# Kernel tuning notes

Measured on AMD Instinct MI355X. Metric: run time of the kernel, lower is better.

## Reference

```python
import jax, jax.numpy as jnp
import numpy as np
from jax import lax

_K1 = np.array([[0,0,0,0,0],[0,-1,2,-1,0],[0,2,4,2,0],[0,-1,2,-1,0],[0,0,0,0,0]], dtype=np.float32)
_K2 = np.array([[-1,2,-2,2,-1],[2,-6,8,-6,2],[-2,8,-12,8,-2],[2,-6,8,-6,2],[-1,2,-2,2,-1]], dtype=np.float32)
_K3 = np.array([[0,0,0,0,0],[0,0,0,0,0],[0,1,-2,1,0],[0,0,0,0,0],[0,0,0,0,0]], dtype=np.float32)

def _depthwise_filter(k, C):
    # OIHW with feature_group_count=C -> (C, 1, 5, 5)
    return jnp.broadcast_to(jnp.asarray(k)[None, None], (C, 1, 5, 5))

def _dwconv(x, f):
    C = x.shape[1]
    return lax.conv_general_dilated(
        x, f, window_strides=(1, 1), padding=[(2, 2), (2, 2)],
        dimension_numbers=('NCHW', 'OIHW', 'NCHW'), feature_group_count=C)

def setup_inputs() -> dict:
    key = jax.random.key(0)
    x = jax.random.normal(key, (64, 3, 512, 512), dtype=jnp.float32)
    return {"x": x}

def reference(x):
    C = x.shape[1]
    f1 = _depthwise_filter(_K1, C)
    f2 = _depthwise_filter(_K2, C)
    f3 = _depthwise_filter(_K3, C)
    edge = _dwconv(x, f1)
    texture = _dwconv(edge, f2)
    residual = _dwconv(texture, f3)
    return residual
```

## Files before the change

### kernel.cpp

```cpp
#include <hip/hip_runtime.h>


#define H 512
#define W 512
#define RS 16
#define STRIPS (H/RS)
#define LOG2_STRIPS 5

typedef float v4f __attribute__((ext_vector_type(4)));

__global__ __launch_bounds__(256, 4)
void resid_kernel(const float* __restrict__ x, float* __restrict__ out) {
    const int lane  = threadIdx.x & 63;
    const int wid   = (blockIdx.x << 2) | (threadIdx.x >> 6);
    const int plane = wid >> LOG2_STRIPS;
    const int strip = wid & (STRIPS - 1);
    const int r0    = strip * RS;
    const int cb    = lane << 3;

    const float* __restrict__ xp = x + (size_t)plane * (H * W);
    float* __restrict__ op = out + (size_t)plane * (H * W);

    float E0[8], E1[8], E2[8], E3[8], E4[8];
    float a0[8], a1[8];
    #pragma unroll
    for (int j = 0; j < 8; ++j) {
        E0[j] = E1[j] = E2[j] = E3[j] = E4[j] = 0.f;
        a0[j] = a1[j] = 0.f;
    }

    for (int r = r0 - 3; r <= r0 + RS + 3; ++r) {
        float v[8], vl, vh;
        if (r >= 0 && r < H) {
            const float4* pr = (const float4*)(xp + r * W + cb);
            float4 qa = pr[0], qb = pr[1];
            v[0] = qa.x; v[1] = qa.y; v[2] = qa.z; v[3] = qa.w;
            v[4] = qb.x; v[5] = qb.y; v[6] = qb.z; v[7] = qb.w;
            vl = (lane > 0)  ? xp[r * W + cb - 1] : 0.f;
            vh = (lane < 63) ? xp[r * W + cb + 8] : 0.f;
        } else {
            #pragma unroll
            for (int j = 0; j < 8; ++j) v[j] = 0.f;
            vl = 0.f; vh = 0.f;
        }

        if (r >= r0 + 4) {
            const int p = r - 4;
            float A[8], B[8];
            #pragma unroll
            for (int j = 0; j < 8; ++j) {
                A[j] = E0[j] - 2.f*E1[j] + 2.f*E2[j] - 2.f*E3[j] + E4[j];
                B[j] = E1[j] - 2.f*E2[j] + E3[j];
            }
            float al1 = __shfl_up(A[7], 1, 64);
            float al2 = __shfl_up(A[6], 1, 64);
            float ah1 = __shfl_down(A[0], 1, 64);
            float ah2 = __shfl_down(A[1], 1, 64);
            float bl  = __shfl_up(B[7], 1, 64);
            float bh  = __shfl_down(B[0], 1, 64);
            if (lane == 0)  { al1 = 0.f; al2 = 0.f; bl = 0.f; }
            if (lane == 63) { ah1 = 0.f; ah2 = 0.f; bh = 0.f; }
            float T[8];
            #pragma unroll
            for (int j = 0; j < 8; ++j) {
                float am2 = (j >= 2) ? A[j-2] : ((j == 1) ? al1 : al2);
                float am1 = (j >= 1) ? A[j-1] : al1;
                float ap1 = (j <= 6) ? A[j+1] : ah1;
                float ap2 = (j <= 5) ? A[j+2] : ((j == 6) ? ah1 : ah2);
                float bm  = (j >= 1) ? B[j-1] : bl;
                float bp  = (j <= 6) ? B[j+1] : bh;
                float lt = am2 - 2.f*am1 + 2.f*A[j] - 2.f*ap1 + ap2;
                float mt = bm - 2.f*B[j] + bp;
                T[j] = -lt - 2.f*mt;
            }
            float tl = __shfl_up(T[7], 1, 64);
            float th = __shfl_down(T[0], 1, 64);
            if (lane == 0)  tl = 0.f;
            if (lane == 63) th = 0.f;
            float R[8];
            #pragma unroll
            for (int j = 0; j < 8; ++j) {
                float tm = (j >= 1) ? T[j-1] : tl;
                float tp = (j <= 6) ? T[j+1] : th;
                R[j] = tm - 2.f*T[j] + tp;
            }
            v4f o0 = { R[0], R[1], R[2], R[3] };
            v4f o1 = { R[4], R[5], R[6], R[7] };
            float* dst = op + p * W + cb;
            __builtin_nontemporal_store(o0, (v4f*)(dst));
            __builtin_nontemporal_store(o1, (v4f*)(dst + 4));
        }

        const bool ein = (r - 1 >= 0) && (r - 1 < H);
        #pragma unroll
        for (int j = 0; j < 8; ++j) {
            float xm = (j >= 1) ? v[j-1] : vl;
            float xq = (j <= 6) ? v[j+1] : vh;
            float h1 = 2.f*v[j] - xm - xq;
            float h2 = 8.f*v[j] - 2.f*h1;
            float En = ein ? (a0[j] + h1) : 0.f;
            a0[j] = a1[j] + h2;
            a1[j] = h1;
            E0[j] = E1[j]; E1[j] = E2[j]; E2[j] = E3[j]; E3[j] = E4[j]; E4[j] = En;
        }
    }
}

extern "C" void kernel_launch(void* const* d_in, const int* in_sizes, int n_in,
                              void* d_out, int out_size, void* d_ws, size_t ws_size,
                              hipStream_t stream) {
    const float* x = (const float*)d_in[0];
    float* out = (float*)d_out;
    resid_kernel<<<dim3(1536), dim3(256), 0, stream>>>(x, out);
}
```

Measured before the change: 361.6 us.

## Fully unroll row loop into four-row groups with batched clamped loads

Replaces the per-row loop with a prologue and four unrolled groups of four rows. Each group issues all four row loads before computing, so more memory requests are in flight per wave. Loads now use clamped, branch-free row addresses and zero the values with selects instead of branching. The register-shifting E window is replaced by ping-pong register sets, and launch bounds drop from 4 to 3 to allow the extra registers, which lowers the occupancy floor.

```diff
diff --git a/kernel.cpp b/kernel.cpp
--- a/kernel.cpp
+++ b/kernel.cpp
@@ -9,7 +9,102 @@
 
 typedef float v4f __attribute__((ext_vector_type(4)));
 
-__global__ __launch_bounds__(256, 4)
+__device__ __forceinline__ void load_row(const float* __restrict__ xp, int r, int cb, int lane,
+                                         float v[8], float& lo, float& hi) {
+    int rc = r; if (rc < 0) rc = 0; if (rc > H - 1) rc = H - 1;
+    const float* rp = xp + rc * W;
+    v4f a = *(const v4f*)(rp + cb);
+    v4f b = *(const v4f*)(rp + cb + 4);
+    float l = rp[(lane == 0)  ? 0       : cb - 1];
+    float h = rp[(lane == 63) ? W - 1   : cb + 8];
+    const bool ok = (r >= 0) && (r < H);
+    v[0] = ok ? a.x : 0.f; v[1] = ok ? a.y : 0.f; v[2] = ok ? a.z : 0.f; v[3] = ok ? a.w : 0.f;
+    v[4] = ok ? b.x : 0.f; v[5] = ok ? b.y : 0.f; v[6] = ok ? b.z : 0.f; v[7] = ok ? b.w : 0.f;
+    lo = (ok && lane > 0)  ? l : 0.f;
+    hi = (ok && lane < 63) ? h : 0.f;
+}
+
+#define FOLD(xv, xl, xh, r, Eout, KEEP)                                   \
+  {                                                                       \
+    const bool eok = ((r) - 1 >= 0) && ((r) - 1 < H);                     \
+    _Pragma("unroll")                                                     \
+    for (int j = 0; j < 8; ++j) {                                         \
+      float xm = (j >= 1) ? xv[j-1] : xl;                                 \
+      float xq = (j <= 6) ? xv[j+1] : xh;                                 \
+      float h1 = 2.f*xv[j] - xm - xq;                                     \
+      float h2 = 8.f*xv[j] - 2.f*h1;                                      \
+      if (KEEP) Eout[j] = eok ? (a0[j] + h1) : 0.f;                       \
+      a0[j] = a1[j] + h2;                                                 \
+      a1[j] = h1;                                                         \
+    }                                                                     \
+  }
+
+#define OUTROW(p, Em2, Em1, Ez, Ep1, Ep2)                                 \
+  {                                                                       \
+    float A[8], B[8];                                                     \
+    _Pragma("unroll")                                                     \
+    for (int j = 0; j < 8; ++j) {                                         \
+      A[j] = Em2[j] - 2.f*Em1[j] + 2.f*Ez[j] - 2.f*Ep1[j] + Ep2[j];       \
+      B[j] = Em1[j] - 2.f*Ez[j] + Ep1[j];                                 \
+    }                                                                     \
+    float al1 = __shfl_up(A[7], 1, 64);                                   \
+    float al2 = __shfl_up(A[6], 1, 64);                                   \
+    float ah1 = __shfl_down(A[0], 1, 64);                                 \
+    float ah2 = __shfl_down(A[1], 1, 64);                                 \
+    float bl  = __shfl_up(B[7], 1, 64);                                   \
+    float bh  = __shfl_down(B[0], 1, 64);                                 \
+    if (lane == 0)  { al1 = 0.f; al2 = 0.f; bl = 0.f; }                   \
+    if (lane == 63) { ah1 = 0.f; ah2 = 0.f; bh = 0.f; }                   \
+    float T[8];                                                           \
+    _Pragma("unroll")                                                     \
+    for (int j = 0; j < 8; ++j) {                                         \
+      float am2 = (j >= 2) ? A[j-2] : ((j == 1) ? al1 : al2);             \
+      float am1 = (j >= 1) ? A[j-1] : al1;                                \
+      float ap1 = (j <= 6) ? A[j+1] : ah1;                                \
+      float ap2 = (j <= 5) ? A[j+2] : ((j == 6) ? ah1 : ah2);             \
+      float bm  = (j >= 1) ? B[j-1] : bl;                                 \
+      float bp  = (j <= 6) ? B[j+1] : bh;                                 \
+      float lt = am2 - 2.f*am1 + 2.f*A[j] - 2.f*ap1 + ap2;                \
+      float mt = bm - 2.f*B[j] + bp;                                      \
+      T[j] = -lt - 2.f*mt;                                                \
+    }                                                                     \
+    float tl = __shfl_up(T[7], 1, 64);                                    \
+    float th = __shfl_down(T[0], 1, 64);                                  \
+    if (lane == 0)  tl = 0.f;                                             \
+    if (lane == 63) th = 0.f;                                             \
+    float Rr[8];                                                          \
+    _Pragma("unroll")                                                     \
+    for (int j = 0; j < 8; ++j) {                                         \
+      float tm = (j >= 1) ? T[j-1] : tl;                                  \
+      float tp = (j <= 6) ? T[j+1] : th;                                  \
+      Rr[j] = tm - 2.f*T[j] + tp;                                         \
+    }                                                                     \
+    v4f o0 = { Rr[0], Rr[1], Rr[2], Rr[3] };                              \
+    v4f o1 = { Rr[4], Rr[5], Rr[6], Rr[7] };                              \
+    float* dst = op + (p) * W + cb;                                       \
+    __builtin_nontemporal_store(o0, (v4f*)(dst));                         \
+    __builtin_nontemporal_store(o1, (v4f*)(dst + 4));                     \
+  }
+
+#define GROUP(P, Oa, Ob, Oc, Od, Na, Nb, Nc, Nd)                          \
+  {                                                                       \
+    float xv0[8], xv1[8], xv2[8], xv3[8];                                 \
+    float xl0, xh0, xl1, xh1, xl2, xh2, xl3, xh3;                         \
+    load_row(xp, (P)+3, cb, lane, xv0, xl0, xh0);                         \
+    load_row(xp, (P)+4, cb, lane, xv1, xl1, xh1);                         \
+    load_row(xp, (P)+5, cb, lane, xv2, xl2, xh2);                         \
+    load_row(xp, (P)+6, cb, lane, xv3, xl3, xh3);                         \
+    FOLD(xv0, xl0, xh0, (P)+3, Na, true);                                 \
+    FOLD(xv1, xl1, xh1, (P)+4, Nb, true);                                 \
+    FOLD(xv2, xl2, xh2, (P)+5, Nc, true);                                 \
+    FOLD(xv3, xl3, xh3, (P)+6, Nd, true);                                 \
+    OUTROW((P),   Oa, Ob, Oc, Od, Na);                                    \
+    OUTROW((P)+1, Ob, Oc, Od, Na, Nb);                                    \
+    OUTROW((P)+2, Oc, Od, Na, Nb, Nc);                                    \
+    OUTROW((P)+3, Od, Na, Nb, Nc, Nd);                                    \
+  }
+
+__global__ __launch_bounds__(256, 3)
 void resid_kernel(const float* __restrict__ x, float* __restrict__ out) {
     const int lane  = threadIdx.x & 63;
     const int wid   = (blockIdx.x << 2) | (threadIdx.x >> 6);
@@ -21,89 +116,34 @@
     const float* __restrict__ xp = x + (size_t)plane * (H * W);
     float* __restrict__ op = out + (size_t)plane * (H * W);
 
-    float E0[8], E1[8], E2[8], E3[8], E4[8];
     float a0[8], a1[8];
     #pragma unroll
-    for (int j = 0; j < 8; ++j) {
-        E0[j] = E1[j] = E2[j] = E3[j] = E4[j] = 0.f;
-        a0[j] = a1[j] = 0.f;
+    for (int j = 0; j < 8; ++j) { a0[j] = 0.f; a1[j] = 0.f; }
+
+    float O0[8], O1[8], O2[8], O3[8];
+    float N0[8], N1[8], N2[8], N3[8];
+
+    {
+        float pv0[8], pv1[8], pv2[8], pv3[8], pv4[8], pv5[8];
+        float pl0, ph0, pl1, ph1, pl2, ph2, pl3, ph3, pl4, ph4, pl5, ph5;
+        load_row(xp, r0-3, cb, lane, pv0, pl0, ph0);
+        load_row(xp, r0-2, cb, lane, pv1, pl1, ph1);
+        load_row(xp, r0-1, cb, lane, pv2, pl2, ph2);
+        load_row(xp, r0,   cb, lane, pv3, pl3, ph3);
+        load_row(xp, r0+1, cb, lane, pv4, pl4, ph4);
+        load_row(xp, r0+2, cb, lane, pv5, pl5, ph5);
+        FOLD(pv0, pl0, ph0, r0-3, O0, false);
+        FOLD(pv1, pl1, ph1, r0-2, O0, false);
+        FOLD(pv2, pl2, ph2, r0-1, O0, true);
+        FOLD(pv3, pl3, ph3, r0,   O1, true);
+        FOLD(pv4, pl4, ph4, r0+1, O2, true);
+        FOLD(pv5, pl5, ph5, r0+2, O3, true);
     }
 
-    for (int r = r0 - 3; r <= r0 + RS + 3; ++r) {
-        float v[8], vl, vh;
-        if (r >= 0 && r < H) {
-            const float4* pr = (const float4*)(xp + r * W + cb);
-            float4 qa = pr[0], qb = pr[1];
-            v[0] = qa.x; v[1] = qa.y; v[2] = qa.z; v[3] = qa.w;
-            v[4] = qb.x; v[5] = qb.y; v[6] = qb.z; v[7] = qb.w;
-            vl = (lane > 0)  ? xp[r * W + cb - 1] : 0.f;
-            vh = (lane < 63) ? xp[r * W + cb + 8] : 0.f;
-        } else {
-            #pragma unroll
-            for (int j = 0; j < 8; ++j) v[j] = 0.f;
-            vl = 0.f; vh = 0.f;
-        }
-
-        if (r >= r0 + 4) {
-            const int p = r - 4;
-            float A[8], B[8];
-            #pragma unroll
-            for (int j = 0; j < 8; ++j) {
-                A[j] = E0[j] - 2.f*E1[j] + 2.f*E2[j] - 2.f*E3[j] + E4[j];
-                B[j] = E1[j] - 2.f*E2[j] + E3[j];
-            }
-            float al1 = __shfl_up(A[7], 1, 64);
-            float al2 = __shfl_up(A[6], 1, 64);
-            float ah1 = __shfl_down(A[0], 1, 64);
-            float ah2 = __shfl_down(A[1], 1, 64);
-            float bl  = __shfl_up(B[7], 1, 64);
-            float bh  = __shfl_down(B[0], 1, 64);
-            if (lane == 0)  { al1 = 0.f; al2 = 0.f; bl = 0.f; }
-            if (lane == 63) { ah1 = 0.f; ah2 = 0.f; bh = 0.f; }
-            float T[8];
-            #pragma unroll
-            for (int j = 0; j < 8; ++j) {
-                float am2 = (j >= 2) ? A[j-2] : ((j == 1) ? al1 : al2);
-                float am1 = (j >= 1) ? A[j-1] : al1;
-                float ap1 = (j <= 6) ? A[j+1] : ah1;
-                float ap2 = (j <= 5) ? A[j+2] : ((j == 6) ? ah1 : ah2);
-                float bm  = (j >= 1) ? B[j-1] : bl;
-                float bp  = (j <= 6) ? B[j+1] : bh;
-                float lt = am2 - 2.f*am1 + 2.f*A[j] - 2.f*ap1 + ap2;
-                float mt = bm - 2.f*B[j] + bp;
-                T[j] = -lt - 2.f*mt;
-            }
-            float tl = __shfl_up(T[7], 1, 64);
-            float th = __shfl_down(T[0], 1, 64);
-            if (lane == 0)  tl = 0.f;
-            if (lane == 63) th = 0.f;
-            float R[8];
-            #pragma unroll
-            for (int j = 0; j < 8; ++j) {
-                float tm = (j >= 1) ? T[j-1] : tl;
-                float tp = (j <= 6) ? T[j+1] : th;
-                R[j] = tm - 2.f*T[j] + tp;
-            }
-            v4f o0 = { R[0], R[1], R[2], R[3] };
-            v4f o1 = { R[4], R[5], R[6], R[7] };
-            float* dst = op + p * W + cb;
-            __builtin_nontemporal_store(o0, (v4f*)(dst));
-            __builtin_nontemporal_store(o1, (v4f*)(dst + 4));
-        }
-
-        const bool ein = (r - 1 >= 0) && (r - 1 < H);
-        #pragma unroll
-        for (int j = 0; j < 8; ++j) {
-            float xm = (j >= 1) ? v[j-1] : vl;
-            float xq = (j <= 6) ? v[j+1] : vh;
-            float h1 = 2.f*v[j] - xm - xq;
-            float h2 = 8.f*v[j] - 2.f*h1;
-            float En = ein ? (a0[j] + h1) : 0.f;
-            a0[j] = a1[j] + h2;
-            a1[j] = h1;
-            E0[j] = E1[j]; E1[j] = E2[j]; E2[j] = E3[j]; E3[j] = E4[j]; E4[j] = En;
-        }
-    }
+    GROUP(r0,      O0, O1, O2, O3, N0, N1, N2, N3);
+    GROUP(r0 + 4,  N0, N1, N2, N3, O0, O1, O2, O3);
+    GROUP(r0 + 8,  O0, O1, O2, O3, N0, N1, N2, N3);
+    GROUP(r0 + 12, N0, N1, N2, N3, O0, O1, O2, O3);
 }
 
 extern "C" void kernel_launch(void* const* d_in, const int* in_sizes, int n_in,
```

Measured after the change: 425.4 us. 17.6% more time.
